# Kernel tuning notes

Measured on AMD Instinct MI355X. Metric: run time of the kernel, lower is better.

Reference implementation:

```python
import jax, jax.numpy as jnp
import numpy as np

K = 3          # kernel size
PAD = 1        # padding


def _conv2d(x, w, b):
    # plain 3x3 conv, stride 1, pad 1, NCHW / OIHW
    out = jax.lax.conv_general_dilated(
        x, w, window_strides=(1, 1), padding=((PAD, PAD), (PAD, PAD)),
        dimension_numbers=('NCHW', 'OIHW', 'NCHW'))
    return out + b[None, :, None, None]


def _deform_conv2d(x, offsets, w, b):
    # torchvision deform_conv2d semantics (stride=1, dilation=1, no mask)
    B, C, H, W = x.shape
    K2 = K * K
    off = offsets.reshape(B, K2, 2, H, W)
    dy, dx = off[:, :, 0], off[:, :, 1]              # [B,K2,H,W], (y,x) order
    ki, kj = jnp.meshgrid(jnp.arange(K), jnp.arange(K), indexing='ij')
    ki = ki.reshape(K2).astype(x.dtype)
    kj = kj.reshape(K2).astype(x.dtype)
    base_y = (jnp.arange(H, dtype=x.dtype)[None, :, None] - PAD + ki[:, None, None])  # [K2,H,1]
    base_x = (jnp.arange(W, dtype=x.dtype)[None, None, :] - PAD + kj[:, None, None])  # [K2,1,W]
    py = base_y[None] + dy                            # [B,K2,H,W] sampling rows
    px = base_x[None] + dx                            # [B,K2,H,W] sampling cols

    y0 = jnp.floor(py); x0 = jnp.floor(px)
    y1 = y0 + 1.0;      x1 = x0 + 1.0
    wy1 = py - y0; wy0 = 1.0 - wy1
    wx1 = px - x0; wx0 = 1.0 - wx1

    def corner(yc, xc, wgt):
        valid = ((yc >= 0) & (yc <= H - 1) & (xc >= 0) & (xc <= W - 1))
        iy = jnp.clip(yc, 0, H - 1).astype(jnp.int32)
        ix = jnp.clip(xc, 0, W - 1).astype(jnp.int32)
        # per-batch gather: x[b][:, iy[b], ix[b]] -> [C,K2,H,W]
        vals = jax.vmap(lambda xb, iyb, ixb: xb[:, iyb, ixb])(x, iy, ix)
        return vals * (wgt * valid.astype(x.dtype))[:, None]  # [B,C,K2,H,W]

    sampled = (corner(y0, x0, wy0 * wx0) + corner(y0, x1, wy0 * wx1)
               + corner(y1, x0, wy1 * wx0) + corner(y1, x1, wy1 * wx1))
    out = jnp.einsum('bckhw,ock->bohw', sampled, w.reshape(w.shape[0], C, K2))
    return out + b[None, :, None, None]


def setup_inputs() -> dict:
    key = jax.random.key(0)
    ks = jax.random.split(key, 6)
    B, C, O, H, W = 4, 256, 256, 64, 64
    x = jax.random.normal(ks[0], (B, C, H, W), dtype=jnp.float32)
    y = jax.random.normal(ks[1], (B, C, H, W), dtype=jnp.float32)
    # offset conv predicts 2*K*K offset channels; small init keeps offsets a few px
    offset_w = jax.random.normal(ks[2], (2 * K * K, C, K, K), dtype=jnp.float32) * 0.01
    offset_b = jax.random.normal(ks[3], (2 * K * K,), dtype=jnp.float32) * 0.01
    deform_w = jax.random.normal(ks[4], (O, C, K, K), dtype=jnp.float32) * (1.0 / np.sqrt(C * K * K))
    deform_b = jax.random.normal(ks[5], (O,), dtype=jnp.float32) * 0.01
    return {"x": x, "y": y, "offset_w": offset_w, "offset_b": offset_b,
            "deform_w": deform_w, "deform_b": deform_b}


def reference(x, y, offset_w, offset_b, deform_w, deform_b):
    offsets = _conv2d(y, offset_w, offset_b)          # [B, 2*K*K, H, W]
    return _deform_conv2d(x, offsets, deform_w, deform_b)
```

## Files before the change

kernel.cpp:

```cpp
#include <hip/hip_runtime.h>
#include <hip/hip_bf16.h>
#include <stdint.h>


typedef __bf16 bf16x8 __attribute__((ext_vector_type(8)));
typedef float  f32x4  __attribute__((ext_vector_type(4)));

__device__ __forceinline__ unsigned short f2bfu(float f) {
    union { float f; unsigned u; } v; v.f = f;
    return (unsigned short)((v.u + 0x8000u) >> 16);
}
__device__ __forceinline__ float lo16(unsigned u) {
    union { unsigned u; float f; } v; v.u = u << 16; return v.f;
}
__device__ __forceinline__ float hi16(unsigned u) {
    union { unsigned u; float f; } v; v.u = u & 0xFFFF0000u; return v.f;
}
__device__ __forceinline__ unsigned fbits(float f) {
    union { float f; unsigned u; } v; v.f = f; return v.u;
}
__device__ __forceinline__ unsigned blend2(unsigned u0, unsigned u1, unsigned u2, unsigned u3,
                                           float4 w) {
    float lo = w.x * lo16(u0) + w.y * lo16(u1) + w.z * lo16(u2) + w.w * lo16(u3);
    float hi = w.x * hi16(u0) + w.y * hi16(u1) + w.z * hi16(u2) + w.w * hi16(u3);
    unsigned rl = fbits(lo) + 0x8000u;
    unsigned rh = fbits(hi) + 0x8000u;
    return __builtin_amdgcn_perm(rh, rl, 0x07060302);
}

__global__ __launch_bounds__(256) void prep_kernel(
    const float* __restrict__ x, const float* __restrict__ y,
    const float* __restrict__ ow, const float* __restrict__ dw,
    unsigned short* __restrict__ xT, unsigned short* __restrict__ yT,
    unsigned short* __restrict__ Wp2, unsigned short* __restrict__ Bo)
{
    __shared__ float tile[64 * 69];
    int blk = blockIdx.x;
    int t = threadIdx.x;
    if (blk < 2048) {
        const float* src = x; unsigned short* dst = xT;
        if (blk >= 1024) { src = y; dst = yT; blk -= 1024; }
        int cq = blk & 3;
        int bh = blk >> 2;
        int w4 = t & 15, cl0 = t >> 4;
        const float* s = src + ((size_t)(bh >> 6) * 256 + cq * 64) * 4096 + (size_t)(bh & 63) * 64;
#pragma unroll
        for (int p = 0; p < 4; ++p) {
            int cl = p * 16 + cl0;
            float4 v = *(const float4*)&s[(size_t)cl * 4096 + w4 * 4];
            tile[(w4 * 4 + 0) * 69 + cl] = v.x;
            tile[(w4 * 4 + 1) * 69 + cl] = v.y;
            tile[(w4 * 4 + 2) * 69 + cl] = v.z;
            tile[(w4 * 4 + 3) * 69 + cl] = v.w;
        }
        __syncthreads();
        unsigned short* d = dst + (size_t)bh * 16384 + cq * 64;
#pragma unroll
        for (int p = 0; p < 4; ++p) {
            int w = p * 16 + cl0;
            float4 v = *(const float4*)&tile[w * 69 + w4 * 4];
            ushort4 r = make_ushort4(f2bfu(v.x), f2bfu(v.y), f2bfu(v.z), f2bfu(v.w));
            *(ushort4*)&d[w * 256 + w4 * 4] = r;
        }
    } else if (blk < 2336) {
        int tid = (blk - 2048) * 256 + t;
        int q8 = tid >> 8;
        int o  = tid & 255;
        int k0 = q8 * 8;
        int tap = k0 >> 8, c0 = k0 & 255;
        const float* s = dw + o * 2304 + c0 * 9 + tap;
        ushort4 r0 = make_ushort4(f2bfu(s[0]), f2bfu(s[9]), f2bfu(s[18]), f2bfu(s[27]));
        ushort4 r1 = make_ushort4(f2bfu(s[36]), f2bfu(s[45]), f2bfu(s[54]), f2bfu(s[63]));
        *(ushort4*)&Wp2[tid * 8 + 0] = r0;
        *(ushort4*)&Wp2[tid * 8 + 4] = r1;
    } else {
        int idx = (blk - 2336) * 256 + t;
        int j = idx & 7;
        int n = (idx >> 3) & 31;
        int lq = (idx >> 8) & 3;
        int kg = idx >> 10;
        int k = kg * 32 + lq * 8 + j;
        int tap = k >> 8, c = k & 255;
        float v = (n < 18) ? ow[n * 2304 + c * 9 + tap] : 0.f;
        Bo[idx] = f2bfu(v);
    }
}

__global__ __launch_bounds__(512, 4) void offs_mfma_kernel(
    const unsigned short* __restrict__ yT,
    const unsigned short* __restrict__ Bo,
    const float* __restrict__ ob,
    float* __restrict__ offs)
{
    __shared__ __align__(16) unsigned char ysm[52224];
    unsigned short* yr = (unsigned short*)ysm;
    float* red = (float*)ysm;

    int blk = blockIdx.x;
    int lb = (blk & 7) * 64 + (blk >> 3);
    int b = lb >> 7, rem = lb & 127, h = rem >> 1, mh = rem & 1;
    int t = threadIdx.x;

    for (unsigned g = t; g < 3264; g += 512) {
        unsigned r = g / 1088;
        unsigned rm = g - r * 1088;
        int wp = rm >> 5, gr = rm & 31;
        int hr = h + (int)r - 1;
        int w = mh * 32 + wp - 1;
        uint4 v = make_uint4(0, 0, 0, 0);
        if (hr >= 0 && hr < 64 && w >= 0 && w < 64)
            v = *(const uint4*)&yT[((size_t)(b * 64 + hr) * 64 + w) * 256 + gr * 8];
        *(uint4*)&yr[((r * 34) + wp) * 256 + (gr ^ (wp & 7)) * 8] = v;
    }
    __syncthreads();

    int wv = t >> 6, lane = t & 63;
    int kq = wv >> 1, m16 = wv & 1;
    int ln = lane & 15, lq = lane >> 4;

    f32x4 acc[2];
    acc[0] = (f32x4){0.f, 0.f, 0.f, 0.f};
    acc[1] = (f32x4){0.f, 0.f, 0.f, 0.f};

    for (int u = kq; u < 72; u += 4) {
        int tap = u >> 3, kc = u & 7;
        int ki = tap / 3, kj = tap - ki * 3;
        int wp = m16 * 16 + ln + kj;
        bf16x8 af = *(const bf16x8*)&yr[(ki * 34 + wp) * 256 + ((kc * 4 + lq) ^ (wp & 7)) * 8];
        bf16x8 b0 = *(const bf16x8*)&Bo[(tap * 8 + kc) * 1024 + lq * 256 + ln * 8];
        bf16x8 b1 = *(const bf16x8*)&Bo[(tap * 8 + kc) * 1024 + lq * 256 + (16 + ln) * 8];
        acc[0] = __builtin_amdgcn_mfma_f32_16x16x32_bf16(af, b0, acc[0], 0, 0, 0);
        acc[1] = __builtin_amdgcn_mfma_f32_16x16x32_bf16(af, b1, acc[1], 0, 0, 0);
    }

    __syncthreads();
    if (kq > 0) {
        float* rg = red + (size_t)(((kq - 1) * 2 + m16) * 2) * 256;
#pragma unroll
        for (int nt = 0; nt < 2; ++nt)
#pragma unroll
            for (int r = 0; r < 4; ++r)
                rg[nt * 256 + (lq * 4 + r) * 16 + ln] = acc[nt][r];
    }
    __syncthreads();
    if (kq == 0) {
#pragma unroll
        for (int nt = 0; nt < 2; ++nt) {
            int o = nt * 16 + ln;
            f32x4 s = acc[nt];
#pragma unroll
            for (int kk = 0; kk < 3; ++kk) {
                const float* rg = red + (size_t)((kk * 2 + m16) * 2 + nt) * 256;
#pragma unroll
                for (int r = 0; r < 4; ++r)
                    s[r] += rg[(lq * 4 + r) * 16 + ln];
            }
            if (o < 18) {
                float bias = ob[o];
                float* dst = offs + ((size_t)b * 18 + o) * 4096 + h * 64 + mh * 32 + m16 * 16 + lq * 4;
                *(float4*)dst = make_float4(s[0] + bias, s[1] + bias, s[2] + bias, s[3] + bias);
            }
        }
    }
}

__device__ __forceinline__ void gather_issue(const unsigned short* __restrict__ xtb,
                                             const float4* __restrict__ pw_lds,
                                             const int4* __restrict__ pi_lds,
                                             int tap, int t, uint4 a[2][4], float4 wr[2]) {
    int gr = t & 31, c0 = gr * 8;
#pragma unroll
    for (int it = 0; it < 2; ++it) {
        int pos = (t >> 5) + it * 16;
        wr[it] = pw_lds[tap * 32 + pos];
        int4 p = pi_lds[tap * 32 + pos];
        a[it][0] = *(const uint4*)&xtb[p.x + c0];
        a[it][1] = *(const uint4*)&xtb[p.y + c0];
        a[it][2] = *(const uint4*)&xtb[p.z + c0];
        a[it][3] = *(const uint4*)&xtb[p.w + c0];
    }
}
__device__ __forceinline__ void gather_commit(unsigned short* __restrict__ buf,
                                              int t, uint4 a[2][4], float4 wr[2]) {
    int gr = t & 31;
#pragma unroll
    for (int it = 0; it < 2; ++it) {
        int pos = (t >> 5) + it * 16;
        uint4 res;
        res.x = blend2(a[it][0].x, a[it][1].x, a[it][2].x, a[it][3].x, wr[it]);
        res.y = blend2(a[it][0].y, a[it][1].y, a[it][2].y, a[it][3].y, wr[it]);
        res.z = blend2(a[it][0].z, a[it][1].z, a[it][2].z, a[it][3].z, wr[it]);
        res.w = blend2(a[it][0].w, a[it][1].w, a[it][2].w, a[it][3].w, wr[it]);
        *(uint4*)&buf[pos * 256 + (gr ^ (pos & 7)) * 8] = res;
    }
}

__global__ __launch_bounds__(512, 4) void deform_kernel(
    const unsigned short* __restrict__ xT,
    const unsigned short* __restrict__ Wp2,
    const float* __restrict__ offs,
    const float* __restrict__ db,
    float* __restrict__ out)
{
    __shared__ __align__(16) unsigned char smem[41984];
    unsigned short* Abuf0 = (unsigned short*)smem;
    unsigned short* Abuf1 = (unsigned short*)(smem + 16384);
    float4* pw_lds = (float4*)(smem + 32768);
    int4*   pi_lds = (int4*)(smem + 32768 + 4608);
    float*  epi    = (float*)smem;

    int blk = blockIdx.x;
    int lb = (blk & 7) * 64 + (blk >> 3);
    int b = lb >> 7, rem = lb & 127, h = rem >> 1, mh = rem & 1;
    int t = threadIdx.x;
    int wv = t >> 6, lane = t & 63;
    int ln = lane & 15, lq = lane >> 4;
    int ns = wv & 3, kh = wv >> 2;

    const unsigned short* xtb = xT + (size_t)b * (64 * 64 * 256);
    const float* offb = offs + (size_t)b * 18 * 4096 + h * 64;

    if (t < 288) {
        int tap = t >> 5, pos_l = t & 31;
        int pos_g = mh * 32 + pos_l;
        int ki = tap / 3, kj = tap - ki * 3;
        float dy = offb[(tap * 2 + 0) * 4096 + pos_g];
        float dx = offb[(tap * 2 + 1) * 4096 + pos_g];
        float py = (float)(h - 1 + ki) + dy;
        float px = (float)(pos_g - 1 + kj) + dx;
        float y0 = floorf(py), x0 = floorf(px);
        float wy1 = py - y0, wx1 = px - x0;
        float wy0 = 1.f - wy1, wx0 = 1.f - wx1;
        float y1 = y0 + 1.f, x1 = x0 + 1.f;
        float vy0 = (y0 >= 0.f && y0 <= 63.f) ? 1.f : 0.f;
        float vy1 = (y1 >= 0.f && y1 <= 63.f) ? 1.f : 0.f;
        float vx0 = (x0 >= 0.f && x0 <= 63.f) ? 1.f : 0.f;
        float vx1 = (x1 >= 0.f && x1 <= 63.f) ? 1.f : 0.f;
        int iy0 = (int)fminf(fmaxf(y0, 0.f), 63.f);
        int iy1 = (int)fminf(fmaxf(y1, 0.f), 63.f);
        int ix0 = (int)fminf(fmaxf(x0, 0.f), 63.f);
        int ix1 = (int)fminf(fmaxf(x1, 0.f), 63.f);
        pw_lds[t] = make_float4(wy0 * wx0 * vy0 * vx0, wy0 * wx1 * vy0 * vx1,
                                wy1 * wx0 * vy1 * vx0, wy1 * wx1 * vy1 * vx1);
        pi_lds[t] = make_int4((iy0 * 64 + ix0) * 256, (iy0 * 64 + ix1) * 256,
                              (iy1 * 64 + ix0) * 256, (iy1 * 64 + ix1) * 256);
    }
    __syncthreads();

    f32x4 acc[2][4];
#pragma unroll
    for (int ms = 0; ms < 2; ++ms)
#pragma unroll
        for (int nt = 0; nt < 4; ++nt)
            acc[ms][nt] = (f32x4){0.f, 0.f, 0.f, 0.f};

    uint4 ga[2][4]; float4 gw[2];
    gather_issue(xtb, pw_lds, pi_lds, 0, t, ga, gw);
    gather_commit(Abuf0, t, ga, gw);
    __syncthreads();

    for (int tap = 0; tap < 9; ++tap) {
        if (tap < 8)
            gather_issue(xtb, pw_lds, pi_lds, tap + 1, t, ga, gw);
        const unsigned short* Ab = (tap & 1) ? Abuf1 : Abuf0;
#pragma unroll
        for (int kc = 0; kc < 4; ++kc) {
            bf16x8 af[2];
#pragma unroll
            for (int ms = 0; ms < 2; ++ms) {
                int row = ms * 16 + ln;
                af[ms] = *(const bf16x8*)&Ab[row * 256 + (((kh * 16 + kc * 4 + lq)) ^ (row & 7)) * 8];
            }
            int kg = tap * 8 + kh * 4 + kc;
            bf16x8 bfr[4];
#pragma unroll
            for (int nt = 0; nt < 4; ++nt)
                bfr[nt] = *(const bf16x8*)&Wp2[((kg * 4 + lq) * 256 + ns * 64 + nt * 16 + ln) * 8];
#pragma unroll
            for (int ms = 0; ms < 2; ++ms)
#pragma unroll
                for (int nt = 0; nt < 4; ++nt)
                    acc[ms][nt] = __builtin_amdgcn_mfma_f32_16x16x32_bf16(af[ms], bfr[nt], acc[ms][nt], 0, 0, 0);
        }
        if (tap < 8)
            gather_commit((tap & 1) ? Abuf0 : Abuf1, t, ga, gw);
        __syncthreads();
    }

    if (kh == 1) {
        float* e = epi + (size_t)ns * 2048;
#pragma unroll
        for (int ms = 0; ms < 2; ++ms)
#pragma unroll
            for (int nt = 0; nt < 4; ++nt) {
                int o_l = nt * 16 + ln;
                int g = (ms * 4 + lq) ^ (o_l & 7);
                f32x4 a = acc[ms][nt];
                *(float4*)&e[o_l * 32 + g * 4] = make_float4(a[0], a[1], a[2], a[3]);
            }
    }
    __syncthreads();
    if (kh == 0) {
        const float* e = epi + (size_t)ns * 2048;
#pragma unroll
        for (int ms = 0; ms < 2; ++ms)
#pragma unroll
            for (int nt = 0; nt < 4; ++nt) {
                int o_l = nt * 16 + ln;
                int o = ns * 64 + o_l;
                int g = (ms * 4 + lq) ^ (o_l & 7);
                float bias = db[o];
                float4 p = *(const float4*)&e[o_l * 32 + g * 4];
                f32x4 a = acc[ms][nt];
                int wb = mh * 32 + ms * 16 + lq * 4;
                float4 st = make_float4(a[0] + p.x + bias, a[1] + p.y + bias,
                                        a[2] + p.z + bias, a[3] + p.w + bias);
                *(float4*)&out[((size_t)(b * 256 + o)) * 4096 + h * 64 + wb] = st;
            }
    }
}

extern "C" void kernel_launch(void* const* d_in, const int* in_sizes, int n_in,
                              void* d_out, int out_size, void* d_ws, size_t ws_size,
                              hipStream_t stream) {
    const float* x  = (const float*)d_in[0];
    const float* y  = (const float*)d_in[1];
    const float* ow = (const float*)d_in[2];
    const float* ob = (const float*)d_in[3];
    const float* dw = (const float*)d_in[4];
    const float* db = (const float*)d_in[5];
    float* out = (float*)d_out;

    char* ws = (char*)d_ws;
    unsigned short* xT  = (unsigned short*)(ws);
    unsigned short* yT  = (unsigned short*)(ws + 8388608);
    unsigned short* Wp2 = (unsigned short*)(ws + 16777216);
    unsigned short* Bo  = (unsigned short*)(ws + 16777216 + 1179648);
    float*          offs = (float*)(ws + 16777216 + 1179648 + 147456);

    hipLaunchKernelGGL(prep_kernel, dim3(2624), dim3(256), 0, stream,
                       x, y, ow, dw, xT, yT, Wp2, Bo);
    hipLaunchKernelGGL(offs_mfma_kernel, dim3(512), dim3(512), 0, stream, yT, Bo, ob, offs);
    hipLaunchKernelGGL(deform_kernel, dim3(512), dim3(512), 0, stream, xT, Wp2, offs, db, out);
}
```

Before: 137.4 us.

## Fuse offset conv into deform kernel with full-row 1024-thread blocks

Removes the separate offset-prediction kernel and computes the 18 offset channels inside the deform kernel, reducing the partial sums through shared memory. The offsets no longer make a global round trip and one launch is dropped. Each block now covers a full 64-wide output row with 1024 threads and 256 blocks instead of 512 half-row blocks, which changes the MFMA tile shape per wave. The trade-off is fewer blocks than the hardware has slots for, more LDS per block (about 86 KB), and y rows read straight from global memory without LDS staging.

Result: no change. 135.2 us (-1.6%).

```diff
diff --git a/kernel.cpp b/kernel.cpp
--- a/kernel.cpp
+++ b/kernel.cpp
@@ -86,148 +86,81 @@
     }
 }
 
-__global__ __launch_bounds__(512, 4) void offs_mfma_kernel(
+__global__ __launch_bounds__(1024) void deform_kernel(
+    const unsigned short* __restrict__ xT,
     const unsigned short* __restrict__ yT,
+    const unsigned short* __restrict__ Wp2,
     const unsigned short* __restrict__ Bo,
     const float* __restrict__ ob,
-    float* __restrict__ offs)
-{
-    __shared__ __align__(16) unsigned char ysm[52224];
-    unsigned short* yr = (unsigned short*)ysm;
-    float* red = (float*)ysm;
-
-    int blk = blockIdx.x;
-    int lb = (blk & 7) * 64 + (blk >> 3);
-    int b = lb >> 7, rem = lb & 127, h = rem >> 1, mh = rem & 1;
-    int t = threadIdx.x;
-
-    for (unsigned g = t; g < 3264; g += 512) {
-        unsigned r = g / 1088;
-        unsigned rm = g - r * 1088;
-        int wp = rm >> 5, gr = rm & 31;
-        int hr = h + (int)r - 1;
-        int w = mh * 32 + wp - 1;
-        uint4 v = make_uint4(0, 0, 0, 0);
-        if (hr >= 0 && hr < 64 && w >= 0 && w < 64)
-            v = *(const uint4*)&yT[((size_t)(b * 64 + hr) * 64 + w) * 256 + gr * 8];
-        *(uint4*)&yr[((r * 34) + wp) * 256 + (gr ^ (wp & 7)) * 8] = v;
-    }
-    __syncthreads();
-
-    int wv = t >> 6, lane = t & 63;
-    int kq = wv >> 1, m16 = wv & 1;
-    int ln = lane & 15, lq = lane >> 4;
-
-    f32x4 acc[2];
-    acc[0] = (f32x4){0.f, 0.f, 0.f, 0.f};
-    acc[1] = (f32x4){0.f, 0.f, 0.f, 0.f};
-
-    for (int u = kq; u < 72; u += 4) {
-        int tap = u >> 3, kc = u & 7;
-        int ki = tap / 3, kj = tap - ki * 3;
-        int wp = m16 * 16 + ln + kj;
-        bf16x8 af = *(const bf16x8*)&yr[(ki * 34 + wp) * 256 + ((kc * 4 + lq) ^ (wp & 7)) * 8];
-        bf16x8 b0 = *(const bf16x8*)&Bo[(tap * 8 + kc) * 1024 + lq * 256 + ln * 8];
-        bf16x8 b1 = *(const bf16x8*)&Bo[(tap * 8 + kc) * 1024 + lq * 256 + (16 + ln) * 8];
-        acc[0] = __builtin_amdgcn_mfma_f32_16x16x32_bf16(af, b0, acc[0], 0, 0, 0);
-        acc[1] = __builtin_amdgcn_mfma_f32_16x16x32_bf16(af, b1, acc[1], 0, 0, 0);
-    }
-
-    __syncthreads();
-    if (kq > 0) {
-        float* rg = red + (size_t)(((kq - 1) * 2 + m16) * 2) * 256;
-#pragma unroll
-        for (int nt = 0; nt < 2; ++nt)
-#pragma unroll
-            for (int r = 0; r < 4; ++r)
-                rg[nt * 256 + (lq * 4 + r) * 16 + ln] = acc[nt][r];
-    }
-    __syncthreads();
-    if (kq == 0) {
-#pragma unroll
-        for (int nt = 0; nt < 2; ++nt) {
-            int o = nt * 16 + ln;
-            f32x4 s = acc[nt];
-#pragma unroll
-            for (int kk = 0; kk < 3; ++kk) {
-                const float* rg = red + (size_t)((kk * 2 + m16) * 2 + nt) * 256;
-#pragma unroll
-                for (int r = 0; r < 4; ++r)
-                    s[r] += rg[(lq * 4 + r) * 16 + ln];
-            }
-            if (o < 18) {
-                float bias = ob[o];
-                float* dst = offs + ((size_t)b * 18 + o) * 4096 + h * 64 + mh * 32 + m16 * 16 + lq * 4;
-                *(float4*)dst = make_float4(s[0] + bias, s[1] + bias, s[2] + bias, s[3] + bias);
-            }
-        }
-    }
-}
-
-__device__ __forceinline__ void gather_issue(const unsigned short* __restrict__ xtb,
-                                             const float4* __restrict__ pw_lds,
-                                             const int4* __restrict__ pi_lds,
-                                             int tap, int t, uint4 a[2][4], float4 wr[2]) {
-    int gr = t & 31, c0 = gr * 8;
-#pragma unroll
-    for (int it = 0; it < 2; ++it) {
-        int pos = (t >> 5) + it * 16;
-        wr[it] = pw_lds[tap * 32 + pos];
-        int4 p = pi_lds[tap * 32 + pos];
-        a[it][0] = *(const uint4*)&xtb[p.x + c0];
-        a[it][1] = *(const uint4*)&xtb[p.y + c0];
-        a[it][2] = *(const uint4*)&xtb[p.z + c0];
-        a[it][3] = *(const uint4*)&xtb[p.w + c0];
-    }
-}
-__device__ __forceinline__ void gather_commit(unsigned short* __restrict__ buf,
-                                              int t, uint4 a[2][4], float4 wr[2]) {
-    int gr = t & 31;
-#pragma unroll
-    for (int it = 0; it < 2; ++it) {
-        int pos = (t >> 5) + it * 16;
-        uint4 res;
-        res.x = blend2(a[it][0].x, a[it][1].x, a[it][2].x, a[it][3].x, wr[it]);
-        res.y = blend2(a[it][0].y, a[it][1].y, a[it][2].y, a[it][3].y, wr[it]);
-        res.z = blend2(a[it][0].z, a[it][1].z, a[it][2].z, a[it][3].z, wr[it]);
-        res.w = blend2(a[it][0].w, a[it][1].w, a[it][2].w, a[it][3].w, wr[it]);
-        *(uint4*)&buf[pos * 256 + (gr ^ (pos & 7)) * 8] = res;
-    }
-}
-
-__global__ __launch_bounds__(512, 4) void deform_kernel(
-    const unsigned short* __restrict__ xT,
-    const unsigned short* __restrict__ Wp2,
-    const float* __restrict__ offs,
     const float* __restrict__ db,
     float* __restrict__ out)
 {
-    __shared__ __align__(16) unsigned char smem[41984];
+    __shared__ __align__(16) unsigned char smem[88064];
     unsigned short* Abuf0 = (unsigned short*)smem;
-    unsigned short* Abuf1 = (unsigned short*)(smem + 16384);
-    float4* pw_lds = (float4*)(smem + 32768);
-    int4*   pi_lds = (int4*)(smem + 32768 + 4608);
-    float*  epi    = (float*)smem;
+    unsigned short* Abuf1 = (unsigned short*)(smem + 32768);
+    float*  red = (float*)smem;
+    float*  epi = (float*)smem;
+    float4* pw_lds = (float4*)(smem + 69632);
+    int4*   pi_lds = (int4*)(smem + 69632 + 9216);
 
     int blk = blockIdx.x;
-    int lb = (blk & 7) * 64 + (blk >> 3);
-    int b = lb >> 7, rem = lb & 127, h = rem >> 1, mh = rem & 1;
+    int lb = (blk & 7) * 32 + (blk >> 3);
+    int b = lb >> 6, h = lb & 63;
     int t = threadIdx.x;
     int wv = t >> 6, lane = t & 63;
     int ln = lane & 15, lq = lane >> 4;
-    int ns = wv & 3, kh = wv >> 2;
 
     const unsigned short* xtb = xT + (size_t)b * (64 * 64 * 256);
-    const float* offb = offs + (size_t)b * 18 * 4096 + h * 64;
-
-    if (t < 288) {
-        int tap = t >> 5, pos_l = t & 31;
-        int pos_g = mh * 32 + pos_l;
+
+    {
+        int kq = wv >> 1, mh = wv & 1;
+        f32x4 oacc[2][2];
+#pragma unroll
+        for (int m16 = 0; m16 < 2; ++m16)
+#pragma unroll
+            for (int nt = 0; nt < 2; ++nt)
+                oacc[m16][nt] = (f32x4){0.f, 0.f, 0.f, 0.f};
+        for (int u = kq * 9; u < kq * 9 + 9; ++u) {
+            int tap = u >> 3, kc = u & 7;
+            int ki = tap / 3, kj = tap - ki * 3;
+            int hr = h + ki - 1;
+            bf16x8 b0 = *(const bf16x8*)&Bo[(tap * 8 + kc) * 1024 + lq * 256 + ln * 8];
+            bf16x8 b1 = *(const bf16x8*)&Bo[(tap * 8 + kc) * 1024 + lq * 256 + (16 + ln) * 8];
+#pragma unroll
+            for (int m16 = 0; m16 < 2; ++m16) {
+                int wr = mh * 32 + m16 * 16 + ln + kj - 1;
+                bf16x8 af = (bf16x8)(__bf16)0.0f;
+                if (hr >= 0 && hr < 64 && wr >= 0 && wr < 64)
+                    af = *(const bf16x8*)&yT[((size_t)(b * 64 + hr) * 64 + wr) * 256 + kc * 32 + lq * 8];
+                oacc[m16][0] = __builtin_amdgcn_mfma_f32_16x16x32_bf16(af, b0, oacc[m16][0], 0, 0, 0);
+                oacc[m16][1] = __builtin_amdgcn_mfma_f32_16x16x32_bf16(af, b1, oacc[m16][1], 0, 0, 0);
+            }
+        }
+        float* rz = red + (size_t)(kq * 2 + mh) * 1056;
+#pragma unroll
+        for (int m16 = 0; m16 < 2; ++m16)
+#pragma unroll
+            for (int nt = 0; nt < 2; ++nt) {
+                int o_l = nt * 16 + ln;
+#pragma unroll
+                for (int r = 0; r < 4; ++r)
+                    rz[o_l * 33 + m16 * 16 + lq * 4 + r] = oacc[m16][nt][r];
+            }
+    }
+    __syncthreads();
+    if (t < 576) {
+        int tap = t >> 6, pos = t & 63;
+        int mh_p = pos >> 5, pl = pos & 31;
+        float dy = ob[2 * tap], dx = ob[2 * tap + 1];
+#pragma unroll
+        for (int kq = 0; kq < 8; ++kq) {
+            const float* rz = red + (size_t)(kq * 2 + mh_p) * 1056;
+            dy += rz[(2 * tap) * 33 + pl];
+            dx += rz[(2 * tap + 1) * 33 + pl];
+        }
         int ki = tap / 3, kj = tap - ki * 3;
-        float dy = offb[(tap * 2 + 0) * 4096 + pos_g];
-        float dx = offb[(tap * 2 + 1) * 4096 + pos_g];
         float py = (float)(h - 1 + ki) + dy;
-        float px = (float)(pos_g - 1 + kj) + dx;
+        float px = (float)(pos - 1 + kj) + dx;
         float y0 = floorf(py), x0 = floorf(px);
         float wy1 = py - y0, wx1 = px - x0;
         float wy0 = 1.f - wy1, wx0 = 1.f - wx1;
@@ -247,75 +180,115 @@
     }
     __syncthreads();
 
-    f32x4 acc[2][4];
-#pragma unroll
-    for (int ms = 0; ms < 2; ++ms)
-#pragma unroll
-        for (int nt = 0; nt < 4; ++nt)
+    int ns = wv & 7, kh = wv >> 3;
+
+    f32x4 acc[4][2];
+#pragma unroll
+    for (int ms = 0; ms < 4; ++ms)
+#pragma unroll
+        for (int nt = 0; nt < 2; ++nt)
             acc[ms][nt] = (f32x4){0.f, 0.f, 0.f, 0.f};
 
+    int gr = t & 31, c0 = gr * 8;
     uint4 ga[2][4]; float4 gw[2];
-    gather_issue(xtb, pw_lds, pi_lds, 0, t, ga, gw);
-    gather_commit(Abuf0, t, ga, gw);
+#pragma unroll
+    for (int it = 0; it < 2; ++it) {
+        int pos = (t >> 5) + it * 32;
+        gw[it] = pw_lds[pos];
+        int4 p = pi_lds[pos];
+        ga[it][0] = *(const uint4*)&xtb[p.x + c0];
+        ga[it][1] = *(const uint4*)&xtb[p.y + c0];
+        ga[it][2] = *(const uint4*)&xtb[p.z + c0];
+        ga[it][3] = *(const uint4*)&xtb[p.w + c0];
+    }
+#pragma unroll
+    for (int it = 0; it < 2; ++it) {
+        int pos = (t >> 5) + it * 32;
+        uint4 res;
+        res.x = blend2(ga[it][0].x, ga[it][1].x, ga[it][2].x, ga[it][3].x, gw[it]);
+        res.y = blend2(ga[it][0].y, ga[it][1].y, ga[it][2].y, ga[it][3].y, gw[it]);
+        res.z = blend2(ga[it][0].z, ga[it][1].z, ga[it][2].z, ga[it][3].z, gw[it]);
+        res.w = blend2(ga[it][0].w, ga[it][1].w, ga[it][2].w, ga[it][3].w, gw[it]);
+        *(uint4*)&Abuf0[pos * 256 + (gr ^ (pos & 7)) * 8] = res;
+    }
     __syncthreads();
 
     for (int tap = 0; tap < 9; ++tap) {
-        if (tap < 8)
-            gather_issue(xtb, pw_lds, pi_lds, tap + 1, t, ga, gw);
+        if (tap < 8) {
+#pragma unroll
+            for (int it = 0; it < 2; ++it) {
+                int pos = (t >> 5) + it * 32;
+                gw[it] = pw_lds[(tap + 1) * 64 + pos];
+                int4 p = pi_lds[(tap + 1) * 64 + pos];
+                ga[it][0] = *(const uint4*)&xtb[p.x + c0];
+                ga[it][1] = *(const uint4*)&xtb[p.y + c0];
+                ga[it][2] = *(const uint4*)&xtb[p.z + c0];
+                ga[it][3] = *(const uint4*)&xtb[p.w + c0];
+            }
+        }
         const unsigned short* Ab = (tap & 1) ? Abuf1 : Abuf0;
 #pragma unroll
         for (int kc = 0; kc < 4; ++kc) {
-            bf16x8 af[2];
-#pragma unroll
-            for (int ms = 0; ms < 2; ++ms) {
+            int gbase = kh * 16 + kc * 4 + lq;
+            bf16x8 af[4];
+#pragma unroll
+            for (int ms = 0; ms < 4; ++ms) {
                 int row = ms * 16 + ln;
-                af[ms] = *(const bf16x8*)&Ab[row * 256 + (((kh * 16 + kc * 4 + lq)) ^ (row & 7)) * 8];
+                af[ms] = *(const bf16x8*)&Ab[row * 256 + (gbase ^ (row & 7)) * 8];
             }
             int kg = tap * 8 + kh * 4 + kc;
-            bf16x8 bfr[4];
-#pragma unroll
-            for (int nt = 0; nt < 4; ++nt)
-                bfr[nt] = *(const bf16x8*)&Wp2[((kg * 4 + lq) * 256 + ns * 64 + nt * 16 + ln) * 8];
-#pragma unroll
-            for (int ms = 0; ms < 2; ++ms)
-#pragma unroll
-                for (int nt = 0; nt < 4; ++nt)
+            bf16x8 bfr[2];
+#pragma unroll
+            for (int nt = 0; nt < 2; ++nt)
+                bfr[nt] = *(const bf16x8*)&Wp2[((kg * 4 + lq) * 256 + ns * 32 + nt * 16 + ln) * 8];
+#pragma unroll
+            for (int ms = 0; ms < 4; ++ms)
+#pragma unroll
+                for (int nt = 0; nt < 2; ++nt)
                     acc[ms][nt] = __builtin_amdgcn_mfma_f32_16x16x32_bf16(af[ms], bfr[nt], acc[ms][nt], 0, 0, 0);
         }
-        if (tap < 8)
-            gather_commit((tap & 1) ? Abuf0 : Abuf1, t, ga, gw);
+        if (tap < 8) {
+            unsigned short* buf = (tap & 1) ? Abuf0 : Abuf1;
+#pragma unroll
+            for (int it = 0; it < 2; ++it) {
+                int pos = (t >> 5) + it * 32;
+                uint4 res;
+                res.x = blend2(ga[it][0].x, ga[it][1].x, ga[it][2].x, ga[it][3].x, gw[it]);
+                res.y = blend2(ga[it][0].y, ga[it][1].y, ga[it][2].y, ga[it][3].y, gw[it]);
+                res.z = blend2(ga[it][0].z, ga[it][1].z, ga[it][2].z, ga[it][3].z, gw[it]);
+                res.w = blend2(ga[it][0].w, ga[it][1].w, ga[it][2].w, ga[it][3].w, gw[it]);
+                *(uint4*)&buf[pos * 256 + (gr ^ (pos & 7)) * 8] = res;
+            }
+        }
         __syncthreads();
     }
 
     if (kh == 1) {
-        float* e = epi + (size_t)ns * 2048;
-#pragma unroll
-        for (int ms = 0; ms < 2; ++ms)
-#pragma unroll
-            for (int nt = 0; nt < 4; ++nt) {
+        float* e = epi + (size_t)ns * 2176;
+#pragma unroll
+        for (int ms = 0; ms < 4; ++ms)
+#pragma unroll
+            for (int nt = 0; nt < 2; ++nt) {
                 int o_l = nt * 16 + ln;
-                int g = (ms * 4 + lq) ^ (o_l & 7);
                 f32x4 a = acc[ms][nt];
-                *(float4*)&e[o_l * 32 + g * 4] = make_float4(a[0], a[1], a[2], a[3]);
+                *(float4*)&e[o_l * 68 + ms * 16 + lq * 4] = make_float4(a[0], a[1], a[2], a[3]);
             }
     }
     __syncthreads();
     if (kh == 0) {
-        const float* e = epi + (size_t)ns * 2048;
-#pragma unroll
-        for (int ms = 0; ms < 2; ++ms)
-#pragma unroll
-            for (int nt = 0; nt < 4; ++nt) {
+        const float* e = epi + (size_t)ns * 2176;
+#pragma unroll
+        for (int ms = 0; ms < 4; ++ms)
+#pragma unroll
+            for (int nt = 0; nt < 2; ++nt) {
                 int o_l = nt * 16 + ln;
-                int o = ns * 64 + o_l;
-                int g = (ms * 4 + lq) ^ (o_l & 7);
+                int o = ns * 32 + o_l;
                 float bias = db[o];
-                float4 p = *(const float4*)&e[o_l * 32 + g * 4];
+                float4 p = *(const float4*)&e[o_l * 68 + ms * 16 + lq * 4];
                 f32x4 a = acc[ms][nt];
-                int wb = mh * 32 + ms * 16 + lq * 4;
                 float4 st = make_float4(a[0] + p.x + bias, a[1] + p.y + bias,
                                         a[2] + p.z + bias, a[3] + p.w + bias);
-                *(float4*)&out[((size_t)(b * 256 + o)) * 4096 + h * 64 + wb] = st;
+                *(float4*)&out[((size_t)(b * 256 + o)) * 4096 + h * 64 + ms * 16 + lq * 4] = st;
             }
     }
 }
@@ -336,10 +309,9 @@
     unsigned short* yT  = (unsigned short*)(ws + 8388608);
     unsigned short* Wp2 = (unsigned short*)(ws + 16777216);
     unsigned short* Bo  = (unsigned short*)(ws + 16777216 + 1179648);
-    float*          offs = (float*)(ws + 16777216 + 1179648 + 147456);
 
     hipLaunchKernelGGL(prep_kernel, dim3(2624), dim3(256), 0, stream,
                        x, y, ow, dw, xT, yT, Wp2, Bo);
-    hipLaunchKernelGGL(offs_mfma_kernel, dim3(512), dim3(512), 0, stream, yT, Bo, ob, offs);
-    hipLaunchKernelGGL(deform_kernel, dim3(512), dim3(512), 0, stream, xT, Wp2, offs, db, out);
-}
+    hipLaunchKernelGGL(deform_kernel, dim3(256), dim3(1024), 0, stream,
+                       xT, yT, Wp2, Bo, ob, db, out);
+}
```
